# Kernel optimization log

Measured on AMD Instinct MI355X. Metric: run time of the kernel, lower is better.

Reference implementation:

```python
import jax, jax.numpy as jnp
import numpy as np
import math

QUERY_LEN = 64
VALUES_LEN = 64
NUM_HEADS = 16


def setup_inputs() -> dict:
    key = jax.random.key(0)
    k1, k2, k3, k4 = jax.random.split(key, 4)
    B, G, N = 2, 4, 1024
    D = QUERY_LEN * NUM_HEADS  # 1024
    queries = jax.random.normal(k1, (B, G, N, D), dtype=jnp.float32)
    keys = jax.random.normal(k2, (B, G, N, D), dtype=jnp.float32)
    values = jax.random.normal(k3, (B, G, N, VALUES_LEN * NUM_HEADS), dtype=jnp.float32)
    neuron_bank_connectivity_sub = jax.random.uniform(k4, (1, G, 1, N, N), dtype=jnp.float32)
    return {
        "queries": queries,
        "keys": keys,
        "values": values,
        "neuron_bank_connectivity_sub": neuron_bank_connectivity_sub,
    }


def reference(queries, keys, values, neuron_bank_connectivity_sub):
    B, G, N, _ = queries.shape
    H, dq, dv = NUM_HEADS, QUERY_LEN, VALUES_LEN
    # view last dim as (vec_len, num_heads), move heads forward: [B,G,H,N,d]
    q = queries.reshape(B, G, N, dq, H).transpose(0, 1, 4, 2, 3)
    k = keys.reshape(B, G, N, dq, H).transpose(0, 1, 4, 2, 3)
    v = values.reshape(B, G, N, dv, H).transpose(0, 1, 4, 2, 3)
    scores = jnp.einsum('bghnd,bghmd->bghnm', q, k) / math.sqrt(dq)
    probs = jax.nn.softmax(scores - neuron_bank_connectivity_sub, axis=-1)
    out = jnp.einsum('bghnm,bghmd->bghnd', probs, v)  # [B,G,H,N,dv]
    # Faithful to original: view() applied to the contiguous [B,G,H,N,dv] buffer
    return out.reshape(B, G, N, H * dv)
```

## Files before the change

kernel.cpp:

```cpp
#include <hip/hip_runtime.h>
#include <hip/hip_bf16.h>
#include <math.h>

#define B_ 2
#define G_ 4
#define N_ 1024
#define H_ 16
#define D_ 64
#define BG_ (B_*G_)
#define BGH_ (B_*G_*H_)
#define MK 64
#define LOG2E 1.44269504f
#define QSCALE (0.125f * LOG2E)

typedef __bf16 bf16;
typedef bf16 bf16x8 __attribute__((ext_vector_type(8)));
typedef float f32x4 __attribute__((ext_vector_type(4)));

#define HS 1160
#define NS 72

__global__ __launch_bounds__(256) void transpose_fused(
    const float* __restrict__ q, const float* __restrict__ k, const float* __restrict__ v,
    bf16* __restrict__ qt, bf16* __restrict__ ktb, bf16* __restrict__ vtT)
{
    __shared__ __attribute__((aligned(16))) bf16 lds[16 * HS];
    int bx = blockIdx.x;
    int tensor = bx >> 9;
    int rr = bx & 511;
    int bg = rr >> 6;
    int tile = rr & 63;
    int n0 = tile * 16;
    int t = threadIdx.x;

    const float* src = (tensor == 0) ? q : (tensor == 1) ? k : v;
    float scale = (tensor == 0) ? QSCALE : 1.0f;
    const float* sb = src + (size_t)bg * N_ * 1024 + (size_t)n0 * 1024;

    int h0 = 4 * (t & 3);
    int d  = t >> 2;
    int wbase = h0 * HS + d;
#pragma unroll 4
    for (int i = 0; i < 16; ++i) {
        float4 val = ((const float4*)(sb + (size_t)i * 1024))[t];
        bf16* p = &lds[wbase + i * NS];
        p[0]        = (bf16)(val.x * scale);
        p[HS]       = (bf16)(val.y * scale);
        p[2 * HS]   = (bf16)(val.z * scale);
        p[3 * HS]   = (bf16)(val.w * scale);
    }
    __syncthreads();

    if (tensor < 2) {
        bf16* dst = (tensor == 0) ? qt : ktb;
        int n  = (t >> 3) & 15;
        int db = t & 7;
        int hb = t >> 7;
#pragma unroll
        for (int i = 0; i < 8; ++i) {
            int h = 2 * i + hb;
            bf16x8 vv = *(const bf16x8*)(&lds[h * HS + n * NS + db * 8]);
            *(bf16x8*)(dst + (((size_t)(bg * H_ + h)) * N_ + n0 + n) * D_ + db * 8) = vv;
        }
    } else {
        int dd = t & 63;
        int nc = (t >> 6) & 1;
        int hb = t >> 7;
#pragma unroll
        for (int i = 0; i < 8; ++i) {
            int h = 2 * i + hb;
            bf16x8 vv;
#pragma unroll
            for (int jj = 0; jj < 8; ++jj)
                vv[jj] = lds[h * HS + (nc * 8 + jj) * NS + dd];
            *(bf16x8*)(vtT + (((size_t)(bg * H_ + h)) * D_ + dd) * N_ + n0 + nc * 8) = vv;
        }
    }
}

__global__ __launch_bounds__(256, 2) void flash_kernel(
    const bf16* __restrict__ qt, const bf16* __restrict__ kt, const bf16* __restrict__ vtT,
    const float* __restrict__ bias, float* __restrict__ out)
{
    __shared__ __attribute__((aligned(16))) bf16 k_lds[MK][72];
    __shared__ __attribute__((aligned(16))) bf16 v_lds[D_][72];
    __shared__ __attribute__((aligned(16))) bf16 p_lds[4][32][72];

    int tid  = threadIdx.x;
    int w    = tid >> 6;
    int lane = tid & 63;
    int quad = lane >> 4;
    int col  = lane & 15;

    int bgh = blockIdx.y;
    int n0  = blockIdx.x * 128;
    int g   = (bgh >> 4) & (G_ - 1);

    const bf16* qb0 = qt + ((size_t)bgh * N_ + n0 + w * 32 + col) * D_;
    const bf16* qb1 = qb0 + 16 * D_;
    bf16x8 aq00 = *(const bf16x8*)(qb0 + quad * 8);
    bf16x8 aq01 = *(const bf16x8*)(qb0 + 32 + quad * 8);
    bf16x8 aq10 = *(const bf16x8*)(qb1 + quad * 8);
    bf16x8 aq11 = *(const bf16x8*)(qb1 + 32 + quad * 8);

    f32x4 acc00 = {0,0,0,0}, acc01 = {0,0,0,0}, acc02 = {0,0,0,0}, acc03 = {0,0,0,0};
    f32x4 acc10 = {0,0,0,0}, acc11 = {0,0,0,0}, acc12 = {0,0,0,0}, acc13 = {0,0,0,0};
    float l0[4] = {0,0,0,0}, l1[4] = {0,0,0,0};

    int srow = tid >> 2;
    int j    = tid & 3;
    int jsw  = (j ^ (srow & 3)) * 16;
    const bf16* kp = kt + (size_t)bgh * N_ * D_ + (size_t)srow * D_ + j * 16;
    const bf16* vp = vtT + ((size_t)bgh * D_ + srow) * N_ + j * 16;

    const float* bb = bias + (size_t)g * N_ * N_;
    const float* bb0 = bb + (size_t)(n0 + w * 32 + quad * 4) * N_ + col;
    const float* bb1 = bb0 + (size_t)16 * N_;

    bf16x8 kr0 = *(const bf16x8*)(kp);
    bf16x8 kr1 = *(const bf16x8*)(kp + 8);
    bf16x8 vr0 = *(const bf16x8*)(vp);
    bf16x8 vr1 = *(const bf16x8*)(vp + 8);

    int kofs0 = (quad * 8) ^ ((col & 3) << 4);
    int kofs1 = (32 + quad * 8) ^ ((col & 3) << 4);
    int pofs0 = (quad * 8) ^ ((col >> 2) << 4);
    int pofs1 = (32 + quad * 8) ^ ((col >> 2) << 4);

    for (int m0 = 0; m0 < N_; m0 += MK) {
        __syncthreads();
        *(bf16x8*)(&k_lds[srow][jsw])     = kr0;
        *(bf16x8*)(&k_lds[srow][jsw + 8]) = kr1;
        *(bf16x8*)(&v_lds[srow][jsw])     = vr0;
        *(bf16x8*)(&v_lds[srow][jsw + 8]) = vr1;
        __syncthreads();

        if (m0 + MK < N_) {
            kp += MK * D_;  vp += MK;
            kr0 = *(const bf16x8*)(kp);
            kr1 = *(const bf16x8*)(kp + 8);
            vr0 = *(const bf16x8*)(vp);
            vr1 = *(const bf16x8*)(vp + 8);
        }

        bf16x8 kb[8];
#pragma unroll
        for (int c = 0; c < 4; ++c) {
            kb[2 * c]     = *(const bf16x8*)(&k_lds[c * 16 + col][kofs0]);
            kb[2 * c + 1] = *(const bf16x8*)(&k_lds[c * 16 + col][kofs1]);
        }
        f32x4 z = {0,0,0,0};
        f32x4 s[4];
#pragma unroll
        for (int c = 0; c < 4; ++c) {
            s[c] = __builtin_amdgcn_mfma_f32_16x16x32_bf16(aq00, kb[2 * c], z, 0, 0, 0);
            s[c] = __builtin_amdgcn_mfma_f32_16x16x32_bf16(aq01, kb[2 * c + 1], s[c], 0, 0, 0);
        }
#pragma unroll
        for (int c = 0; c < 4; ++c) {
#pragma unroll
            for (int r = 0; r < 4; ++r) {
                float bv = bb0[(size_t)r * N_ + m0 + c * 16];
                float p = __builtin_amdgcn_exp2f(__builtin_fmaf(-LOG2E, bv, s[c][r]));
                l0[r] += p;
                p_lds[w][quad * 4 + r][((c ^ quad) << 4) + col] = (bf16)p;
            }
        }
#pragma unroll
        for (int c = 0; c < 4; ++c) {
            s[c] = __builtin_amdgcn_mfma_f32_16x16x32_bf16(aq10, kb[2 * c], z, 0, 0, 0);
            s[c] = __builtin_amdgcn_mfma_f32_16x16x32_bf16(aq11, kb[2 * c + 1], s[c], 0, 0, 0);
        }
#pragma unroll
        for (int c = 0; c < 4; ++c) {
#pragma unroll
            for (int r = 0; r < 4; ++r) {
                float bv = bb1[(size_t)r * N_ + m0 + c * 16];
                float p = __builtin_amdgcn_exp2f(__builtin_fmaf(-LOG2E, bv, s[c][r]));
                l1[r] += p;
                p_lds[w][16 + quad * 4 + r][((c ^ quad) << 4) + col] = (bf16)p;
            }
        }

        bf16x8 ap00 = *(const bf16x8*)(&p_lds[w][col][pofs0]);
        bf16x8 ap01 = *(const bf16x8*)(&p_lds[w][col][pofs1]);
        bf16x8 ap10 = *(const bf16x8*)(&p_lds[w][16 + col][pofs0]);
        bf16x8 ap11 = *(const bf16x8*)(&p_lds[w][16 + col][pofs1]);

        bf16x8 bv0 = *(const bf16x8*)(&v_lds[col][kofs0]);
        bf16x8 bv1 = *(const bf16x8*)(&v_lds[col][kofs1]);
        acc00 = __builtin_amdgcn_mfma_f32_16x16x32_bf16(ap00, bv0, acc00, 0, 0, 0);
        acc00 = __builtin_amdgcn_mfma_f32_16x16x32_bf16(ap01, bv1, acc00, 0, 0, 0);
        acc10 = __builtin_amdgcn_mfma_f32_16x16x32_bf16(ap10, bv0, acc10, 0, 0, 0);
        acc10 = __builtin_amdgcn_mfma_f32_16x16x32_bf16(ap11, bv1, acc10, 0, 0, 0);

        bv0 = *(const bf16x8*)(&v_lds[16 + col][kofs0]);
        bv1 = *(const bf16x8*)(&v_lds[16 + col][kofs1]);
        acc01 = __builtin_amdgcn_mfma_f32_16x16x32_bf16(ap00, bv0, acc01, 0, 0, 0);
        acc01 = __builtin_amdgcn_mfma_f32_16x16x32_bf16(ap01, bv1, acc01, 0, 0, 0);
        acc11 = __builtin_amdgcn_mfma_f32_16x16x32_bf16(ap10, bv0, acc11, 0, 0, 0);
        acc11 = __builtin_amdgcn_mfma_f32_16x16x32_bf16(ap11, bv1, acc11, 0, 0, 0);

        bv0 = *(const bf16x8*)(&v_lds[32 + col][kofs0]);
        bv1 = *(const bf16x8*)(&v_lds[32 + col][kofs1]);
        acc02 = __builtin_amdgcn_mfma_f32_16x16x32_bf16(ap00, bv0, acc02, 0, 0, 0);
        acc02 = __builtin_amdgcn_mfma_f32_16x16x32_bf16(ap01, bv1, acc02, 0, 0, 0);
        acc12 = __builtin_amdgcn_mfma_f32_16x16x32_bf16(ap10, bv0, acc12, 0, 0, 0);
        acc12 = __builtin_amdgcn_mfma_f32_16x16x32_bf16(ap11, bv1, acc12, 0, 0, 0);

        bv0 = *(const bf16x8*)(&v_lds[48 + col][kofs0]);
        bv1 = *(const bf16x8*)(&v_lds[48 + col][kofs1]);
        acc03 = __builtin_amdgcn_mfma_f32_16x16x32_bf16(ap00, bv0, acc03, 0, 0, 0);
        acc03 = __builtin_amdgcn_mfma_f32_16x16x32_bf16(ap01, bv1, acc03, 0, 0, 0);
        acc13 = __builtin_amdgcn_mfma_f32_16x16x32_bf16(ap10, bv0, acc13, 0, 0, 0);
        acc13 = __builtin_amdgcn_mfma_f32_16x16x32_bf16(ap11, bv1, acc13, 0, 0, 0);
    }

#pragma unroll
    for (int r = 0; r < 4; ++r) {
#pragma unroll
        for (int off = 1; off <= 8; off <<= 1) {
            l0[r] += __shfl_xor(l0[r], off, 64);
            l1[r] += __shfl_xor(l1[r], off, 64);
        }
    }
#pragma unroll
    for (int r = 0; r < 4; ++r) {
        int rown = n0 + w * 32 + quad * 4 + r;
        float inv = 1.0f / l0[r];
        float* ob = out + ((size_t)bgh * N_ + rown) * D_ + col;
        ob[0]  = acc00[r] * inv;
        ob[16] = acc01[r] * inv;
        ob[32] = acc02[r] * inv;
        ob[48] = acc03[r] * inv;
        inv = 1.0f / l1[r];
        float* ob1 = ob + 16 * D_;
        ob1[0]  = acc10[r] * inv;
        ob1[16] = acc11[r] * inv;
        ob1[32] = acc12[r] * inv;
        ob1[48] = acc13[r] * inv;
    }
}

__global__ __launch_bounds__(256) void naive_kernel(
    const float* __restrict__ q, const float* __restrict__ k,
    const float* __restrict__ v, const float* __restrict__ bias,
    float* __restrict__ out)
{
    __shared__ float sc[N_];
    __shared__ float red[256];
    __shared__ float qrow[64];
    int n = blockIdx.x;
    int bgh = blockIdx.y;
    int bg = bgh >> 4, h = bgh & 15;
    int g = bg & (G_ - 1);
    int tid = threadIdx.x;
    const float* qr = q + ((size_t)(bg * N_ + n)) * 1024;
    if (tid < 64) qrow[tid] = qr[tid * 16 + h];
    __syncthreads();
    const float* bb = bias + (size_t)g * N_ * N_ + (size_t)n * N_;
    for (int m = tid; m < N_; m += 256) {
        const float* kr = k + ((size_t)(bg * N_ + m)) * 1024 + h;
        float dot = 0.f;
        for (int d = 0; d < 64; ++d) dot += qrow[d] * kr[d * 16];
        sc[m] = dot * 0.125f - bb[m];
    }
    __syncthreads();
    float mx = -INFINITY;
    for (int m = tid; m < N_; m += 256) mx = fmaxf(mx, sc[m]);
    red[tid] = mx; __syncthreads();
    for (int s = 128; s > 0; s >>= 1) {
        if (tid < s) red[tid] = fmaxf(red[tid], red[tid + s]);
        __syncthreads();
    }
    float M = red[0]; __syncthreads();
    float sum = 0.f;
    for (int m = tid; m < N_; m += 256) { float e = __expf(sc[m] - M); sc[m] = e; sum += e; }
    red[tid] = sum; __syncthreads();
    for (int s = 128; s > 0; s >>= 1) {
        if (tid < s) red[tid] += red[tid + s];
        __syncthreads();
    }
    float L = red[0]; __syncthreads();
    int d = tid & 63, quarter = tid >> 6;
    float acc = 0.f;
    const float* vb = v + (size_t)bg * N_ * 1024 + d * 16 + h;
    for (int m = quarter * 256; m < quarter * 256 + 256; ++m) acc += sc[m] * vb[(size_t)m * 1024];
    red[tid] = acc; __syncthreads();
    if (tid < 64) {
        float o = (red[tid] + red[tid + 64] + red[tid + 128] + red[tid + 192]) / L;
        out[((size_t)bgh * N_ + n) * 64 + d] = o;
    }
}

extern "C" void kernel_launch(void* const* d_in, const int* in_sizes, int n_in,
                              void* d_out, int out_size, void* d_ws, size_t ws_size,
                              hipStream_t stream) {
    const float* q    = (const float*)d_in[0];
    const float* k    = (const float*)d_in[1];
    const float* v    = (const float*)d_in[2];
    const float* bias = (const float*)d_in[3];
    float* out = (float*)d_out;

    const size_t elems = (size_t)BGH_ * N_ * D_;
    const size_t need  = 3 * elems * sizeof(bf16);

    if (ws_size >= need) {
        bf16* qt  = (bf16*)d_ws;
        bf16* ktb = qt + elems;
        bf16* vtT = ktb + elems;
        transpose_fused<<<3 * 512, 256, 0, stream>>>(q, k, v, qt, ktb, vtT);
        dim3 grid(N_ / 128, BGH_);
        flash_kernel<<<grid, 256, 0, stream>>>(qt, ktb, vtT, bias, out);
    } else {
        dim3 grid(N_, BGH_);
        naive_kernel<<<grid, 256, 0, stream>>>(q, k, v, bias, out);
    }
}
```

Baseline: 234.6 us.

## Keep P in registers via transposed MFMA and double-buffer K/V LDS tiles

```diff
diff --git a/kernel.cpp b/kernel.cpp
--- a/kernel.cpp
+++ b/kernel.cpp
@@ -15,7 +15,23 @@
 
 typedef __bf16 bf16;
 typedef bf16 bf16x8 __attribute__((ext_vector_type(8)));
+typedef bf16 bf16x4 __attribute__((ext_vector_type(4)));
+typedef short s16x4 __attribute__((ext_vector_type(4)));
 typedef float f32x4 __attribute__((ext_vector_type(4)));
+
+#if __has_builtin(__builtin_amdgcn_mfma_f32_16x16x16bf16_1k)
+static __device__ __forceinline__ f32x4 mfma16(bf16x4 a, bf16x4 b, f32x4 c) {
+    return __builtin_amdgcn_mfma_f32_16x16x16bf16_1k(
+        __builtin_bit_cast(s16x4, a), __builtin_bit_cast(s16x4, b), c, 0, 0, 0);
+}
+#else
+static __device__ __forceinline__ f32x4 mfma16(bf16x4 a, bf16x4 b, f32x4 c) {
+    f32x4 d;
+    asm("v_mfma_f32_16x16x16_bf16 %0, %1, %2, %3"
+        : "=v"(d) : "v"(a), "v"(b), "0"(c));
+    return d;
+}
+#endif
 
 #define HS 1160
 #define NS 72
@@ -82,15 +98,16 @@
     const bf16* __restrict__ qt, const bf16* __restrict__ kt, const bf16* __restrict__ vtT,
     const float* __restrict__ bias, float* __restrict__ out)
 {
-    __shared__ __attribute__((aligned(16))) bf16 k_lds[MK][72];
-    __shared__ __attribute__((aligned(16))) bf16 v_lds[D_][72];
-    __shared__ __attribute__((aligned(16))) bf16 p_lds[4][32][72];
+    __shared__ __attribute__((aligned(16))) bf16 k_lds[2][MK][72];
+    __shared__ __attribute__((aligned(16))) bf16 v_lds[2][D_][72];
 
     int tid  = threadIdx.x;
     int w    = tid >> 6;
     int lane = tid & 63;
     int quad = lane >> 4;
     int col  = lane & 15;
+    int c3   = col & 3;
+    int q4   = quad * 4;
 
     int bgh = blockIdx.y;
     int n0  = blockIdx.x * 128;
@@ -103,9 +120,10 @@
     bf16x8 aq10 = *(const bf16x8*)(qb1 + quad * 8);
     bf16x8 aq11 = *(const bf16x8*)(qb1 + 32 + quad * 8);
 
-    f32x4 acc00 = {0,0,0,0}, acc01 = {0,0,0,0}, acc02 = {0,0,0,0}, acc03 = {0,0,0,0};
-    f32x4 acc10 = {0,0,0,0}, acc11 = {0,0,0,0}, acc12 = {0,0,0,0}, acc13 = {0,0,0,0};
-    float l0[4] = {0,0,0,0}, l1[4] = {0,0,0,0};
+    f32x4 acc0[4], acc1[4];
+#pragma unroll
+    for (int t = 0; t < 4; ++t) { acc0[t] = (f32x4){0,0,0,0}; acc1[t] = (f32x4){0,0,0,0}; }
+    float l0 = 0.f, l1 = 0.f;
 
     int srow = tid >> 2;
     int j    = tid & 3;
@@ -113,29 +131,27 @@
     const bf16* kp = kt + (size_t)bgh * N_ * D_ + (size_t)srow * D_ + j * 16;
     const bf16* vp = vtT + ((size_t)bgh * D_ + srow) * N_ + j * 16;
 
-    const float* bb = bias + (size_t)g * N_ * N_;
-    const float* bb0 = bb + (size_t)(n0 + w * 32 + quad * 4) * N_ + col;
-    const float* bb1 = bb0 + (size_t)16 * N_;
+    const float* bbL0 = bias + (size_t)g * N_ * N_ + (size_t)(n0 + w * 32 + col) * N_;
+    const float* bbL1 = bbL0 + (size_t)16 * N_;
 
     bf16x8 kr0 = *(const bf16x8*)(kp);
     bf16x8 kr1 = *(const bf16x8*)(kp + 8);
     bf16x8 vr0 = *(const bf16x8*)(vp);
     bf16x8 vr1 = *(const bf16x8*)(vp + 8);
-
-    int kofs0 = (quad * 8) ^ ((col & 3) << 4);
-    int kofs1 = (32 + quad * 8) ^ ((col & 3) << 4);
-    int pofs0 = (quad * 8) ^ ((col >> 2) << 4);
-    int pofs1 = (32 + quad * 8) ^ ((col >> 2) << 4);
-
-    for (int m0 = 0; m0 < N_; m0 += MK) {
+    *(bf16x8*)(&k_lds[0][srow][jsw])     = kr0;
+    *(bf16x8*)(&k_lds[0][srow][jsw + 8]) = kr1;
+    *(bf16x8*)(&v_lds[0][srow][jsw])     = vr0;
+    *(bf16x8*)(&v_lds[0][srow][jsw + 8]) = vr1;
+
+    int kofs0 = (quad * 8) ^ (c3 << 4);
+    int kofs1 = (32 + quad * 8) ^ (c3 << 4);
+
+    for (int it = 0; it < N_ / MK; ++it) {
+        int m0  = it * MK;
+        int cur = it & 1;
         __syncthreads();
-        *(bf16x8*)(&k_lds[srow][jsw])     = kr0;
-        *(bf16x8*)(&k_lds[srow][jsw + 8]) = kr1;
-        *(bf16x8*)(&v_lds[srow][jsw])     = vr0;
-        *(bf16x8*)(&v_lds[srow][jsw + 8]) = vr1;
-        __syncthreads();
-
-        if (m0 + MK < N_) {
+
+        if (it + 1 < N_ / MK) {
             kp += MK * D_;  vp += MK;
             kr0 = *(const bf16x8*)(kp);
             kr1 = *(const bf16x8*)(kp + 8);
@@ -143,102 +159,71 @@
             vr1 = *(const bf16x8*)(vp + 8);
         }
 
-        bf16x8 kb[8];
+        f32x4 bv0[4], bv1[4];
 #pragma unroll
         for (int c = 0; c < 4; ++c) {
-            kb[2 * c]     = *(const bf16x8*)(&k_lds[c * 16 + col][kofs0]);
-            kb[2 * c + 1] = *(const bf16x8*)(&k_lds[c * 16 + col][kofs1]);
-        }
+            bv0[c] = *(const f32x4*)(bbL0 + m0 + c * 16 + q4);
+            bv1[c] = *(const f32x4*)(bbL1 + m0 + c * 16 + q4);
+        }
+
+        f32x4 s0[4], s1[4];
         f32x4 z = {0,0,0,0};
-        f32x4 s[4];
 #pragma unroll
         for (int c = 0; c < 4; ++c) {
-            s[c] = __builtin_amdgcn_mfma_f32_16x16x32_bf16(aq00, kb[2 * c], z, 0, 0, 0);
-            s[c] = __builtin_amdgcn_mfma_f32_16x16x32_bf16(aq01, kb[2 * c + 1], s[c], 0, 0, 0);
-        }
+            bf16x8 kb0 = *(const bf16x8*)(&k_lds[cur][c * 16 + col][kofs0]);
+            bf16x8 kb1 = *(const bf16x8*)(&k_lds[cur][c * 16 + col][kofs1]);
+            s0[c] = __builtin_amdgcn_mfma_f32_16x16x32_bf16(kb0, aq00, z, 0, 0, 0);
+            s0[c] = __builtin_amdgcn_mfma_f32_16x16x32_bf16(kb1, aq01, s0[c], 0, 0, 0);
+            s1[c] = __builtin_amdgcn_mfma_f32_16x16x32_bf16(kb0, aq10, z, 0, 0, 0);
+            s1[c] = __builtin_amdgcn_mfma_f32_16x16x32_bf16(kb1, aq11, s1[c], 0, 0, 0);
+        }
+
+        bf16x4 pb0[4], pb1[4];
 #pragma unroll
         for (int c = 0; c < 4; ++c) {
 #pragma unroll
             for (int r = 0; r < 4; ++r) {
-                float bv = bb0[(size_t)r * N_ + m0 + c * 16];
-                float p = __builtin_amdgcn_exp2f(__builtin_fmaf(-LOG2E, bv, s[c][r]));
-                l0[r] += p;
-                p_lds[w][quad * 4 + r][((c ^ quad) << 4) + col] = (bf16)p;
+                float p0 = __builtin_amdgcn_exp2f(__builtin_fmaf(-LOG2E, bv0[c][r], s0[c][r]));
+                float p1 = __builtin_amdgcn_exp2f(__builtin_fmaf(-LOG2E, bv1[c][r], s1[c][r]));
+                l0 += p0;  l1 += p1;
+                pb0[c][r] = (bf16)p0;
+                pb1[c][r] = (bf16)p1;
             }
         }
+
 #pragma unroll
         for (int c = 0; c < 4; ++c) {
-            s[c] = __builtin_amdgcn_mfma_f32_16x16x32_bf16(aq10, kb[2 * c], z, 0, 0, 0);
-            s[c] = __builtin_amdgcn_mfma_f32_16x16x32_bf16(aq11, kb[2 * c + 1], s[c], 0, 0, 0);
-        }
-#pragma unroll
-        for (int c = 0; c < 4; ++c) {
-#pragma unroll
-            for (int r = 0; r < 4; ++r) {
-                float bv = bb1[(size_t)r * N_ + m0 + c * 16];
-                float p = __builtin_amdgcn_exp2f(__builtin_fmaf(-LOG2E, bv, s[c][r]));
-                l1[r] += p;
-                p_lds[w][16 + quad * 4 + r][((c ^ quad) << 4) + col] = (bf16)p;
+            int vofs = ((c ^ c3) << 4) + q4;
+#pragma unroll
+            for (int t = 0; t < 4; ++t) {
+                bf16x4 va = *(const bf16x4*)(&v_lds[cur][t * 16 + col][vofs]);
+                acc0[t] = mfma16(va, pb0[c], acc0[t]);
+                acc1[t] = mfma16(va, pb1[c], acc1[t]);
             }
         }
 
-        bf16x8 ap00 = *(const bf16x8*)(&p_lds[w][col][pofs0]);
-        bf16x8 ap01 = *(const bf16x8*)(&p_lds[w][col][pofs1]);
-        bf16x8 ap10 = *(const bf16x8*)(&p_lds[w][16 + col][pofs0]);
-        bf16x8 ap11 = *(const bf16x8*)(&p_lds[w][16 + col][pofs1]);
-
-        bf16x8 bv0 = *(const bf16x8*)(&v_lds[col][kofs0]);
-        bf16x8 bv1 = *(const bf16x8*)(&v_lds[col][kofs1]);
-        acc00 = __builtin_amdgcn_mfma_f32_16x16x32_bf16(ap00, bv0, acc00, 0, 0, 0);
-        acc00 = __builtin_amdgcn_mfma_f32_16x16x32_bf16(ap01, bv1, acc00, 0, 0, 0);
-        acc10 = __builtin_amdgcn_mfma_f32_16x16x32_bf16(ap10, bv0, acc10, 0, 0, 0);
-        acc10 = __builtin_amdgcn_mfma_f32_16x16x32_bf16(ap11, bv1, acc10, 0, 0, 0);
-
-        bv0 = *(const bf16x8*)(&v_lds[16 + col][kofs0]);
-        bv1 = *(const bf16x8*)(&v_lds[16 + col][kofs1]);
-        acc01 = __builtin_amdgcn_mfma_f32_16x16x32_bf16(ap00, bv0, acc01, 0, 0, 0);
-        acc01 = __builtin_amdgcn_mfma_f32_16x16x32_bf16(ap01, bv1, acc01, 0, 0, 0);
-        acc11 = __builtin_amdgcn_mfma_f32_16x16x32_bf16(ap10, bv0, acc11, 0, 0, 0);
-        acc11 = __builtin_amdgcn_mfma_f32_16x16x32_bf16(ap11, bv1, acc11, 0, 0, 0);
-
-        bv0 = *(const bf16x8*)(&v_lds[32 + col][kofs0]);
-        bv1 = *(const bf16x8*)(&v_lds[32 + col][kofs1]);
-        acc02 = __builtin_amdgcn_mfma_f32_16x16x32_bf16(ap00, bv0, acc02, 0, 0, 0);
-        acc02 = __builtin_amdgcn_mfma_f32_16x16x32_bf16(ap01, bv1, acc02, 0, 0, 0);
-        acc12 = __builtin_amdgcn_mfma_f32_16x16x32_bf16(ap10, bv0, acc12, 0, 0, 0);
-        acc12 = __builtin_amdgcn_mfma_f32_16x16x32_bf16(ap11, bv1, acc12, 0, 0, 0);
-
-        bv0 = *(const bf16x8*)(&v_lds[48 + col][kofs0]);
-        bv1 = *(const bf16x8*)(&v_lds[48 + col][kofs1]);
-        acc03 = __builtin_amdgcn_mfma_f32_16x16x32_bf16(ap00, bv0, acc03, 0, 0, 0);
-        acc03 = __builtin_amdgcn_mfma_f32_16x16x32_bf16(ap01, bv1, acc03, 0, 0, 0);
-        acc13 = __builtin_amdgcn_mfma_f32_16x16x32_bf16(ap10, bv0, acc13, 0, 0, 0);
-        acc13 = __builtin_amdgcn_mfma_f32_16x16x32_bf16(ap11, bv1, acc13, 0, 0, 0);
-    }
-
-#pragma unroll
-    for (int r = 0; r < 4; ++r) {
-#pragma unroll
-        for (int off = 1; off <= 8; off <<= 1) {
-            l0[r] += __shfl_xor(l0[r], off, 64);
-            l1[r] += __shfl_xor(l1[r], off, 64);
-        }
-    }
-#pragma unroll
-    for (int r = 0; r < 4; ++r) {
-        int rown = n0 + w * 32 + quad * 4 + r;
-        float inv = 1.0f / l0[r];
-        float* ob = out + ((size_t)bgh * N_ + rown) * D_ + col;
-        ob[0]  = acc00[r] * inv;
-        ob[16] = acc01[r] * inv;
-        ob[32] = acc02[r] * inv;
-        ob[48] = acc03[r] * inv;
-        inv = 1.0f / l1[r];
-        float* ob1 = ob + 16 * D_;
-        ob1[0]  = acc10[r] * inv;
-        ob1[16] = acc11[r] * inv;
-        ob1[32] = acc12[r] * inv;
-        ob1[48] = acc13[r] * inv;
+        if (it + 1 < N_ / MK) {
+            *(bf16x8*)(&k_lds[cur ^ 1][srow][jsw])     = kr0;
+            *(bf16x8*)(&k_lds[cur ^ 1][srow][jsw + 8]) = kr1;
+            *(bf16x8*)(&v_lds[cur ^ 1][srow][jsw])     = vr0;
+            *(bf16x8*)(&v_lds[cur ^ 1][srow][jsw + 8]) = vr1;
+        }
+    }
+
+    l0 += __shfl_xor(l0, 16, 64);
+    l0 += __shfl_xor(l0, 32, 64);
+    l1 += __shfl_xor(l1, 16, 64);
+    l1 += __shfl_xor(l1, 32, 64);
+    float inv0 = 1.0f / l0, inv1 = 1.0f / l1;
+
+    float* ob0 = out + ((size_t)bgh * N_ + n0 + w * 32 + col) * D_ + q4;
+    float* ob1 = ob0 + (size_t)16 * D_;
+#pragma unroll
+    for (int t = 0; t < 4; ++t) {
+        f32x4 o0 = acc0[t] * inv0;
+        f32x4 o1 = acc1[t] * inv1;
+        *(f32x4*)(ob0 + t * 16) = o0;
+        *(f32x4*)(ob1 + t * 16) = o1;
     }
 }
 
```

After: 267.6 us. 1.14x slower.
